# Performance work log

Measured on AMD Instinct MI355X. Metric: run time of the kernel, lower is better.

## Reference

```python
import jax, jax.numpy as jnp
import numpy as np

VAR0, VAR1 = 0.1, 0.2       # variances used by encode()
THRESH = 0.35               # overlap_thresh
NEGPOS = 7                  # negpos_ratio


def point_form(p):
    # (cx,cy,w,h) -> (xmin,ymin,xmax,ymax)
    return jnp.concatenate([p[:, :2] - p[:, 2:] / 2, p[:, :2] + p[:, 2:] / 2], axis=1)


def jaccard(a, b):
    # a:[G,4], b:[P,4] corner form -> IoU [G,P]
    lt = jnp.maximum(a[:, None, :2], b[None, :, :2])
    rb = jnp.minimum(a[:, None, 2:], b[None, :, 2:])
    wh = jnp.clip(rb - lt, 0.0, None)
    inter = wh[..., 0] * wh[..., 1]
    area_a = (a[:, 2] - a[:, 0]) * (a[:, 3] - a[:, 1])
    area_b = (b[:, 2] - b[:, 0]) * (b[:, 3] - b[:, 1])
    return inter / (area_a[:, None] + area_b[None, :] - inter)


def encode(matched, priors):
    g_cxcy = ((matched[:, :2] + matched[:, 2:]) / 2 - priors[:, :2]) / (VAR0 * priors[:, 2:])
    g_wh = jnp.log((matched[:, 2:] - matched[:, :2]) / priors[:, 2:]) / VAR1
    return jnp.concatenate([g_cxcy, g_wh], axis=1)


def encode_landm(matched, priors):
    m = matched.reshape(-1, 5, 2)                                  # [P,5,2]
    g = (m - priors[:, None, :2]) / (VAR0 * priors[:, None, 2:])
    return g.reshape(-1, 10)


def match_one(truths, labels, landms, priors, priors_pf):
    # truths:[G,4] labels:[G] landms:[G,10] priors:[P,4](cxcywh) priors_pf:[P,4](corner)
    G = truths.shape[0]
    P = priors.shape[0]
    ov = jaccard(truths, priors_pf)                                # [G,P]
    best_prior_ov = ov.max(axis=1)                                 # [G]
    best_prior_idx = ov.argmax(axis=1)                             # [G]
    valid_gt = best_prior_ov >= 0.2
    best_truth_ov = ov.max(axis=0)                                 # [P]
    best_truth_idx = ov.argmax(axis=0)                             # [P]
    # index_fill_(0, best_prior_idx[valid_gt], 2): 2 > any IoU, so max is equivalent
    forced_ov = jnp.zeros((P,), ov.dtype).at[best_prior_idx].max(jnp.where(valid_gt, 2.0, 0.0))
    best_truth_ov = jnp.maximum(best_truth_ov, forced_ov)
    forced_idx = jnp.full((P,), -1, jnp.int32).at[best_prior_idx].max(jnp.arange(G, dtype=jnp.int32))
    best_truth_idx = jnp.where(forced_idx >= 0, forced_idx, best_truth_idx.astype(jnp.int32))
    conf = labels[best_truth_idx].astype(jnp.int32)
    conf = jnp.where(best_truth_ov < THRESH, 0, conf)
    loc = encode(truths[best_truth_idx], priors)                   # [P,4]
    landm = encode_landm(landms[best_truth_idx], priors)           # [P,10]
    # if no valid gt, torch zeroes the targets for this sample
    any_valid = valid_gt.any()
    loc = jnp.where(any_valid, loc, 0.0)
    landm = jnp.where(any_valid, landm, 0.0)
    conf = jnp.where(any_valid, conf, 0)
    return loc, conf, landm


def smooth_l1(x):
    ax = jnp.abs(x)
    return jnp.where(ax < 1.0, 0.5 * ax * ax, ax - 0.5)


def setup_inputs() -> dict:
    key = jax.random.key(0)
    k1, k2, k3, k4, k5, k6, k7, k8, k9 = jax.random.split(key, 9)
    B, P, G, C = 64, 16800, 32, 2
    cls_data = jax.random.normal(k1, (B, P, C), jnp.float32)
    loc_data = jax.random.normal(k2, (B, P, 4), jnp.float32)
    landm_data = jax.random.normal(k3, (B, P, 10), jnp.float32)
    # priors in (cx,cy,w,h), w,h in [0.02,0.3]
    pc = jax.random.uniform(k4, (P, 2), jnp.float32)
    pwh = jax.random.uniform(k5, (P, 2), jnp.float32, 0.02, 0.3)
    priors = jnp.concatenate([pc, pwh], axis=1)
    # targets: [B,G,15] = 4 box (corner form, valid) + 10 landmarks + 1 label
    c = jax.random.uniform(k6, (B, G, 2), jnp.float32, 0.15, 0.85)
    s = jax.random.uniform(k7, (B, G, 2), jnp.float32, 0.02, 0.3)
    boxes = jnp.concatenate([c - s / 2, c + s / 2], axis=-1)
    lms = jax.random.uniform(k8, (B, G, 10), jnp.float32)
    labels = jnp.where(jax.random.uniform(k9, (B, G, 1)) < 0.3, -1.0, 1.0)
    targets = jnp.concatenate([boxes, lms, labels], axis=-1)
    return {"cls_data": cls_data, "loc_data": loc_data, "landm_data": landm_data,
            "priors": priors, "targets": targets}


def reference(cls_data, loc_data, landm_data, priors, targets):
    truths = targets[:, :, :4]
    landms = targets[:, :, 4:14]
    labels = targets[:, :, 14]
    priors_pf = point_form(priors)
    loc_t, conf_t, landm_t = jax.vmap(
        lambda t, l, lm: match_one(t, l, lm, priors, priors_pf))(truths, labels, landms)
    num, P = conf_t.shape

    # landmark loss (smooth L1 over conf_t > 0)
    pos1 = conf_t > 0
    N1 = jnp.maximum(pos1.sum().astype(jnp.float32), 1.0)
    loss_landm = jnp.sum(smooth_l1(landm_data - landm_t) * pos1[..., None].astype(landm_data.dtype))

    # localization loss (smooth L1 over conf_t != 0)
    pos = conf_t != 0
    conf_t = jnp.where(pos, 1, conf_t)                              # conf_t[pos] = 1
    loss_l = jnp.sum(smooth_l1(loc_data - loc_t) * pos[..., None].astype(loc_data.dtype))

    # hard negative mining on per-prior CE loss
    logz = jax.nn.logsumexp(cls_data, axis=-1)                      # [B,P]
    gold = jnp.take_along_axis(cls_data, conf_t[..., None], axis=-1)[..., 0]
    loss_c = jnp.where(pos, 0.0, logz - gold)
    loss_idx = jnp.argsort(-loss_c, axis=1)
    idx_rank = jnp.argsort(loss_idx, axis=1)
    num_pos = pos.sum(axis=1, keepdims=True)
    num_neg = jnp.clip(NEGPOS * num_pos, None, P - 1)
    neg = idx_rank < num_neg

    sel = (pos | neg).astype(cls_data.dtype)
    loss_conf = jnp.sum((logz - gold) * sel)

    N = jnp.maximum(num_pos.sum().astype(jnp.float32), 1.0)
    return loss_l / N, loss_conf / N, loss_landm / N1
```

## Files before the change

### kernel.cpp

```cpp
#include <hip/hip_runtime.h>
#include <hip/hip_bf16.h>
#include <math.h>


#define RCP(x) __builtin_amdgcn_rcpf(x)
typedef unsigned long long u64;

constexpr int GN = 32;
constexpr int PACKF = 576;
constexpr int NW64A = 264;

__device__ __forceinline__ float sl1(float x) {
    float a = fabsf(x);
    return a < 1.f ? 0.5f * a * a : a - 0.5f;
}

constexpr int GPB = 4;
constexpr int GNT = 1024;
__global__ __launch_bounds__(GNT)
void k_gt(const float4* __restrict__ priors, const float* __restrict__ targets,
          u64* __restrict__ keys, float* __restrict__ pack, u64* __restrict__ wmask,
          int* __restrict__ done, int P, int G, int NCH) {
    const int b = blockIdx.y, cx = blockIdx.x, g0 = cx * GPB, tid = threadIdx.x;
    const int lane = tid & 63, w = tid >> 6;
    if (cx == 0 && b == 0 && tid == 0) *done = 0;
    __shared__ float4 s_box[GPB];
    __shared__ float  s_at[GPB];
    __shared__ u64 s_wk[GNT / 64][GPB];
    if (tid < GPB) {
        const float* t = targets + ((size_t)b * G + g0 + tid) * 15;
        float4 v = make_float4(t[0], t[1], t[2], t[3]);
        float at = (v.z - v.x) * (v.w - v.y);
        s_box[tid] = v;
        s_at[tid] = at;
        float* pkw = pack + (size_t)b * PACKF;
        ((float4*)pkw)[g0 + tid] = v;
        pkw[128 + g0 + tid] = 0.35f * at;
        pkw[160 + g0 + tid] = at;
        pkw[192 + g0 + tid] = t[14];
    }
    {
        int q = tid - GPB;
        if (q >= 0 && q < GPB * 10) {
            int gg = g0 + q / 10, j = q % 10;
            pack[(size_t)b * PACKF + 224 + gg * 10 + j] =
                targets[((size_t)b * G + gg) * 15 + 4 + j];
        }
    }
    __syncthreads();
    float4 tb0 = s_box[0], tb1 = s_box[1], tb2 = s_box[2], tb3 = s_box[3];
    float at0 = s_at[0], at1 = s_at[1], at2 = s_at[2], at3 = s_at[3];
    float c0 = 0.35f * at0, c1 = 0.35f * at1, c2 = 0.35f * at2, c3 = 0.35f * at3;

    u64* __restrict__ wm = wmask + ((size_t)b * NCH + cx) * NW64A;

    float bv[GPB]; int bp[GPB];
    #pragma unroll
    for (int j = 0; j < GPB; ++j) { bv[j] = -1.f; bp[j] = 0; }

    for (int p = tid; p < P; p += GNT) {
        float4 pr = priors[p];
        float hx = pr.z * 0.5f, hy = pr.w * 0.5f;
        float px0 = pr.x - hx, py0 = pr.y - hy;
        float px1 = pr.x + hx, py1 = pr.y + hy;
        float ap = (px1 - px0) * (py1 - py0);
        float ap35 = 0.35f * ap;
        bool pa = false;
        #pragma unroll
        for (int j = 0; j < GPB; ++j) {
            float4 tb = j == 0 ? tb0 : (j == 1 ? tb1 : (j == 2 ? tb2 : tb3));
            float at = j == 0 ? at0 : (j == 1 ? at1 : (j == 2 ? at2 : at3));
            float cj = j == 0 ? c0 : (j == 1 ? c1 : (j == 2 ? c2 : c3));
            float lx = fmaxf(tb.x, px0), ly = fmaxf(tb.y, py0);
            float rx = fminf(tb.z, px1), ry = fminf(tb.w, py1);
            float iw = fmaxf(rx - lx, 0.f), ih = fmaxf(ry - ly, 0.f);
            float inter = iw * ih;
            pa = pa || (fmaf(1.35f, inter, -cj) >= ap35);
            float iou = inter * RCP(at + ap - inter);
            if (iou > bv[j]) { bv[j] = iou; bp[j] = p; }
        }
        u64 bal = __ballot(pa);
        if (lane == 0) wm[p >> 6] = bal;
    }
    #pragma unroll
    for (int j = 0; j < GPB; ++j) {
        u64 key = ((u64)__float_as_uint(bv[j]) << 32) | ~(unsigned)bp[j];
        #pragma unroll
        for (int o = 32; o > 0; o >>= 1) {
            u64 t = __shfl_down(key, o, 64);
            if (t > key) key = t;
        }
        if (lane == 0) s_wk[w][j] = key;
    }
    __syncthreads();
    if (tid < GPB) {
        u64 m = 0ull;
        #pragma unroll
        for (int q = 0; q < GNT / 64; ++q) { u64 t = s_wk[q][tid]; if (t > m) m = t; }
        keys[b * G + g0 + tid] = m;
    }
}

__global__ __launch_bounds__(256)
void k_match(const float2* __restrict__ cls, const float4* __restrict__ loc,
             const float* __restrict__ lmd, const float4* __restrict__ priors,
             const float* __restrict__ pack, const u64* __restrict__ keys,
             const u64* __restrict__ wmask,
             float* __restrict__ bc, float* __restrict__ part,
             int P, int NB, int NCH) {
    const int b = blockIdx.y, bx = blockIdx.x, tid = threadIdx.x;
    const int lane = tid & 63, w = tid >> 6;
    const float* __restrict__ pk = pack + (size_t)b * PACKF;
    const float4* __restrict__ gbox = (const float4*)pk;
    const float* __restrict__ garea = pk + 160;
    const float* __restrict__ glab = pk + 192;
    const float* __restrict__ glm  = pk + 224;

    __shared__ int s_fg[256];
    __shared__ int s_fv[256];
    __shared__ unsigned s_vm;
    __shared__ float s_red[4][8];

    s_fg[tid] = -1; s_fv[tid] = 0;
    __syncthreads();
    if (tid < GN) {
        u64 key = keys[b * GN + tid];
        unsigned bp = ~(unsigned)key;
        bool val = __uint_as_float((unsigned)(key >> 32)) >= 0.2f;
        u64 bal = __ballot(val);
        if (tid == 0) s_vm = (unsigned)bal;
        int local = (int)bp - bx * 256;
        if (local >= 0 && local < 256) {
            atomicMax(&s_fg[local], tid);
            if (val) atomicOr(&s_fv[local], 1);
        }
    }

    int p = bx * 256 + tid;
    const bool act = p < P;
    float2 c = act ? cls[(size_t)b * P + p] : make_float2(0.f, 0.f);

    const int word = bx * 4 + w;
    u64 m = 0ull;
    #pragma unroll
    for (int ch = 0; ch < 8; ++ch)
        m |= wmask[((size_t)b * NCH + ch) * NW64A + word];
    __syncthreads();
    const bool av = s_vm != 0u;

    bool thr = act && ((m >> lane) & 1ull);
    int fidx = s_fg[tid];
    bool fv = s_fv[tid] != 0;
    bool pos = act && av && (fv || thr);

    float lse = 0.f, d = 0.f;
    if (act) {
        d = c.y - c.x;
        float m0 = fmaxf(d, 0.f);
        lse = m0 + __logf(__expf(-m0) + __expf(d - m0));
        bc[(size_t)b * P + p] = pos ? 0.f : lse;
    }

    float a_ll = 0.f, a_lm = 0.f, a_lcp = 0.f;
    bool posl = false;
    if (pos) {
        a_lcp = lse - d;
        float4 pr = priors[p];
        float hx = pr.z * 0.5f, hy = pr.w * 0.5f;
        float px0 = pr.x - hx, py0 = pr.y - hy;
        float px1 = pr.x + hx, py1 = pr.y + hy;
        float ap = (px1 - px0) * (py1 - py0);
        int bti2 = fidx;
        if (fidx < 0) {
            float btv = -1.f;
            #pragma unroll 1
            for (int g = 0; g < GN; ++g) {
                float4 tb = gbox[g];
                float lx = fmaxf(tb.x, px0), ly = fmaxf(tb.y, py0);
                float rx = fminf(tb.z, px1), ry = fminf(tb.w, py1);
                float iw = fmaxf(rx - lx, 0.f), ih = fmaxf(ry - ly, 0.f);
                float inter = iw * ih;
                float iou = inter * RCP(garea[g] + ap - inter);
                if (iou > btv) { btv = iou; bti2 = g; }
            }
        }
        float4 tb = gbox[bti2];
        float rw = RCP(pr.z), rh = RCP(pr.w);
        float e0 = ((tb.x + tb.z) * 0.5f - pr.x) * rw * 10.f;
        float e1 = ((tb.y + tb.w) * 0.5f - pr.y) * rh * 10.f;
        float e2 = __logf((tb.z - tb.x) * rw) * 5.f;
        float e3 = __logf((tb.w - tb.y) * rh) * 5.f;
        float4 ld = loc[(size_t)b * P + p];
        a_ll = sl1(ld.x - e0) + sl1(ld.y - e1) + sl1(ld.z - e2) + sl1(ld.w - e3);
        if (glab[bti2] > 0.f) {
            posl = true;
            const float* lp = lmd + ((size_t)b * P + p) * 10;
            #pragma unroll
            for (int q = 0; q < 5; ++q) {
                float gx = (glm[bti2 * 10 + 2 * q]     - pr.x) * rw * 10.f;
                float gy = (glm[bti2 * 10 + 2 * q + 1] - pr.y) * rh * 10.f;
                a_lm += sl1(lp[2 * q] - gx) + sl1(lp[2 * q + 1] - gy);
            }
        }
    }

    u64 bpos = __ballot(pos);
    int npw  = __popcll(bpos);
    int np1w = __popcll(__ballot(posl));
    if (bpos) {
        #pragma unroll
        for (int o = 32; o > 0; o >>= 1) {
            a_ll  += __shfl_down(a_ll,  o, 64);
            a_lm  += __shfl_down(a_lm,  o, 64);
            a_lcp += __shfl_down(a_lcp, o, 64);
        }
    }
    if (lane == 0) {
        s_red[w][0] = a_ll; s_red[w][1] = a_lm; s_red[w][2] = a_lcp;
        s_red[w][3] = (float)npw; s_red[w][4] = (float)np1w;
    }
    __syncthreads();
    if (tid == 0) {
        float* pp = part + ((size_t)b * NB + bx) * 8;
        #pragma unroll
        for (int j = 0; j < 5; ++j)
            pp[j] = s_red[0][j] + s_red[1][j] + s_red[2][j] + s_red[3][j];
    }
}

constexpr int KNT = 1024;
constexpr int KNI = 17;
__global__ __launch_bounds__(KNT)
void k_select(const float* __restrict__ bc, const float* __restrict__ part,
              float* __restrict__ part2, float* __restrict__ out,
              int* __restrict__ done, int P, int NB, int B) {
    const int b = blockIdx.x, tid = threadIdx.x;
    const int lane = tid & 63, w = tid >> 6;
    __shared__ float s_r[5];
    __shared__ u64   s_cw[16];
    __shared__ u64   s_ct;
    __shared__ float s_rf[16][2];
    __shared__ float s_ts2[2];
    __shared__ int   s_last;

    unsigned ul[KNI];
    #pragma unroll
    for (int i = 0; i < KNI; ++i) {
        int idx = i * KNT + tid;
        ul[i] = idx < P ? __float_as_uint(bc[(size_t)b * P + idx]) : 0u;
    }
    if (w < 5) {
        float s = 0.f;
        for (int bx = lane; bx < NB; bx += 64) s += part[((size_t)b * NB + bx) * 8 + w];
        #pragma unroll
        for (int o = 32; o > 0; o >>= 1) s += __shfl_down(s, o, 64);
        if (lane == 0) s_r[w] = s;
    }
    __syncthreads();
    const float t_ll = s_r[0], t_lm = s_r[1], t_lcp = s_r[2];
    const float t_np = s_r[3], t_np1 = s_r[4];
    int k = (int)(t_np + 0.5f) * 7;
    if (k > P - 1) k = P - 1;

    float topk = 0.f;
    if (k > 0) {
        unsigned lo = 0u, hi = 0x7f800000u;
        while (lo < hi) {
            unsigned span = hi - lo;
            unsigned m1 = lo + ((span + 3) >> 2);
            unsigned m2 = lo + ((span + 1) >> 1);
            unsigned m3 = hi - (span >> 2);
            int c1 = 0, c2 = 0, c3 = 0;
            #pragma unroll
            for (int i = 0; i < KNI; ++i) {
                unsigned u = ul[i];
                c1 += u >= m1 ? 1 : 0;
                c2 += u >= m2 ? 1 : 0;
                c3 += u >= m3 ? 1 : 0;
            }
            u64 pkk = (u64)c1 | ((u64)c2 << 20) | ((u64)c3 << 40);
            #pragma unroll
            for (int o = 32; o > 0; o >>= 1) pkk += __shfl_down(pkk, o, 64);
            if (lane == 0) s_cw[w] = pkk;
            __syncthreads();
            if (w == 0) {
                u64 t = (lane < 16) ? s_cw[lane] : 0ull;
                #pragma unroll
                for (int o = 8; o > 0; o >>= 1) t += __shfl_down(t, o, 64);
                if (lane == 0) s_ct = t;
            }
            __syncthreads();
            u64 t = s_ct;
            int C1 = (int)(t & 0xFFFFFu);
            int C2 = (int)((t >> 20) & 0xFFFFFu);
            int C3 = (int)((t >> 40) & 0xFFFFFu);
            if      (C3 >= k) lo = m3;
            else if (C2 >= k) { lo = m2; hi = m3 - 1; }
            else if (C1 >= k) { lo = m1; hi = m2 - 1; }
            else hi = m1 - 1;
        }
        float fT = __uint_as_float(lo);
        float s = 0.f, cf = 0.f;
        #pragma unroll
        for (int i = 0; i < KNI; ++i)
            if (ul[i] > lo) { s += __uint_as_float(ul[i]); cf += 1.f; }
        #pragma unroll
        for (int o = 32; o > 0; o >>= 1) {
            s  += __shfl_down(s, o, 64);
            cf += __shfl_down(cf, o, 64);
        }
        if (lane == 0) { s_rf[w][0] = s; s_rf[w][1] = cf; }
        __syncthreads();
        if (w == 0) {
            float a = (lane < 16) ? s_rf[lane][0] : 0.f;
            float bb = (lane < 16) ? s_rf[lane][1] : 0.f;
            #pragma unroll
            for (int o = 8; o > 0; o >>= 1) {
                a  += __shfl_down(a, o, 64);
                bb += __shfl_down(bb, o, 64);
            }
            if (lane == 0) { s_ts2[0] = a; s_ts2[1] = bb; }
        }
        __syncthreads();
        topk = s_ts2[0] + ((float)k - s_ts2[1]) * fT;
    }
    if (tid == 0) {
        float* pp = part2 + b * 8;
        pp[0] = t_ll; pp[1] = t_lm; pp[2] = t_lcp;
        pp[3] = topk; pp[4] = t_np; pp[5] = t_np1;
        __threadfence();
        int old = atomicAdd(done, 1);
        s_last = (old == B - 1) ? 1 : 0;
    }
    __syncthreads();
    if (s_last && w == 0) {
        __threadfence();
        volatile float* vp = part2;
        float ll = 0.f, lm = 0.f, lc = 0.f, tk = 0.f, np = 0.f, np1 = 0.f;
        for (int bb = lane; bb < B; bb += 64) {
            ll  += vp[bb * 8 + 0];
            lm  += vp[bb * 8 + 1];
            lc  += vp[bb * 8 + 2];
            tk  += vp[bb * 8 + 3];
            np  += vp[bb * 8 + 4];
            np1 += vp[bb * 8 + 5];
        }
        #pragma unroll
        for (int o = 32; o > 0; o >>= 1) {
            ll  += __shfl_down(ll,  o, 64);
            lm  += __shfl_down(lm,  o, 64);
            lc  += __shfl_down(lc,  o, 64);
            tk  += __shfl_down(tk,  o, 64);
            np  += __shfl_down(np,  o, 64);
            np1 += __shfl_down(np1, o, 64);
        }
        if (lane == 0) {
            float N = fmaxf(np, 1.f), N1 = fmaxf(np1, 1.f);
            out[0] = ll / N;
            out[1] = (lc + tk) / N;
            out[2] = lm / N1;
        }
    }
}

extern "C" void kernel_launch(void* const* d_in, const int* in_sizes, int n_in,
                              void* d_out, int out_size, void* d_ws, size_t ws_size,
                              hipStream_t stream) {
    const float2* cls    = (const float2*)d_in[0];
    const float4* loc    = (const float4*)d_in[1];
    const float* lmd     = (const float*)d_in[2];
    const float4* priors = (const float4*)d_in[3];
    const float* targets = (const float*)d_in[4];
    int P = in_sizes[3] / 4;
    int B = (in_sizes[1] / 4) / P;
    int G = in_sizes[4] / (15 * B);
    int NB = (P + 255) / 256;
    int NCH = (G + GPB - 1) / GPB;

    size_t off = 0;
    u64* keys    = (u64*)d_ws;                     off += (size_t)B * G * 8;
    u64* wmask   = (u64*)((char*)d_ws + off);      off += (size_t)B * NCH * NW64A * 8;
    float* pack  = (float*)((char*)d_ws + off);    off += (size_t)B * PACKF * 4;
    float* part  = (float*)((char*)d_ws + off);    off += (size_t)B * NB * 8 * 4;
    float* part2 = (float*)((char*)d_ws + off);    off += (size_t)B * 8 * 4;
    int* done    = (int*)((char*)d_ws + off);      off += 256;
    off = (off + 255) & ~(size_t)255;
    float* bc    = (float*)((char*)d_ws + off);

    dim3 ggt(NCH, B);
    k_gt<<<ggt, GNT, 0, stream>>>(priors, targets, keys, pack, wmask, done, P, G, NCH);
    dim3 gm(NB, B);
    k_match<<<gm, 256, 0, stream>>>(cls, loc, lmd, priors, pack, keys, wmask,
                                    bc, part, P, NB, NCH);
    k_select<<<B, KNT, 0, stream>>>(bc, part, part2, (float*)d_out, done, P, NB, B);
}
```

Measured before the change: 89.00 us.

## Fuse three kernels into one cooperative kernel with grid syncs

Replaces the three separate kernel launches (GT matching, per-prior match/loss, top-k selection) with a single cooperative kernel that uses grid.sync between phases. Each batch now gets 4 blocks of 1024 threads handling 8 GTs each and a 4224-prior segment, down from 8 GT chunks and many 256-thread blocks. The aim is to cut launch overhead and inter-kernel gaps. In exchange the grid is much smaller (B*4 blocks), so per-block work and shared-memory use rise, grid syncs add their own cost, and G and the segment size are hardcoded.

```diff
diff --git a/kernel.cpp b/kernel.cpp
--- a/kernel.cpp
+++ b/kernel.cpp
@@ -1,38 +1,59 @@
 #include <hip/hip_runtime.h>
-#include <hip/hip_bf16.h>
+#include <hip/hip_cooperative_groups.h>
 #include <math.h>
 
 
+namespace cg = cooperative_groups;
 #define RCP(x) __builtin_amdgcn_rcpf(x)
 typedef unsigned long long u64;
 
 constexpr int GN = 32;
 constexpr int PACKF = 576;
+constexpr int NCH  = 4;
+constexpr int GPB  = 8;
+constexpr int SEG  = 4224;
 constexpr int NW64A = 264;
+constexpr int NT   = 1024;
+constexpr int NWV  = NT / 64;
 
 __device__ __forceinline__ float sl1(float x) {
     float a = fabsf(x);
     return a < 1.f ? 0.5f * a * a : a - 0.5f;
 }
 
-constexpr int GPB = 4;
-constexpr int GNT = 1024;
-__global__ __launch_bounds__(GNT)
-void k_gt(const float4* __restrict__ priors, const float* __restrict__ targets,
-          u64* __restrict__ keys, float* __restrict__ pack, u64* __restrict__ wmask,
-          int* __restrict__ done, int P, int G, int NCH) {
-    const int b = blockIdx.y, cx = blockIdx.x, g0 = cx * GPB, tid = threadIdx.x;
+__global__ __launch_bounds__(NT)
+void k_fused(const float2* __restrict__ cls, const float4* __restrict__ loc,
+             const float* __restrict__ lmd, const float4* __restrict__ priors,
+             const float* __restrict__ targets,
+             u64* __restrict__ keys, float* __restrict__ pack, u64* __restrict__ wmask,
+             float* __restrict__ bc, float* __restrict__ part, float* __restrict__ part2,
+             float* __restrict__ out, int* __restrict__ done, int P, int B) {
+    cg::grid_group grid = cg::this_grid();
+    const int cb = blockIdx.x, tid = threadIdx.x;
     const int lane = tid & 63, w = tid >> 6;
-    if (cx == 0 && b == 0 && tid == 0) *done = 0;
+    const int b = cb >> 2, sub = cb & 3;
+
     __shared__ float4 s_box[GPB];
     __shared__ float  s_at[GPB];
-    __shared__ u64 s_wk[GNT / 64][GPB];
+    __shared__ u64    s_wk[NWV][GPB];
+    __shared__ int    s_fg[SEG];
+    __shared__ unsigned s_fvb[SEG / 32];
+    __shared__ unsigned s_vm;
+    __shared__ float  s_red[NWV][8];
+    __shared__ float  s_r[5];
+    __shared__ u64    s_cw[NWV];
+    __shared__ u64    s_ct;
+    __shared__ float  s_rf[NWV][2];
+    __shared__ float  s_ts2[2];
+    __shared__ int    s_last;
+
+    if (cb == 0 && tid == 0) *done = 0;
+    const int g0 = sub * GPB;
     if (tid < GPB) {
-        const float* t = targets + ((size_t)b * G + g0 + tid) * 15;
+        const float* t = targets + ((size_t)b * GN + g0 + tid) * 15;
         float4 v = make_float4(t[0], t[1], t[2], t[3]);
         float at = (v.z - v.x) * (v.w - v.y);
-        s_box[tid] = v;
-        s_at[tid] = at;
+        s_box[tid] = v; s_at[tid] = at;
         float* pkw = pack + (size_t)b * PACKF;
         ((float4*)pkw)[g0 + tid] = v;
         pkw[128 + g0 + tid] = 0.35f * at;
@@ -44,21 +65,21 @@
         if (q >= 0 && q < GPB * 10) {
             int gg = g0 + q / 10, j = q % 10;
             pack[(size_t)b * PACKF + 224 + gg * 10 + j] =
-                targets[((size_t)b * G + gg) * 15 + 4 + j];
-        }
-    }
-    __syncthreads();
-    float4 tb0 = s_box[0], tb1 = s_box[1], tb2 = s_box[2], tb3 = s_box[3];
-    float at0 = s_at[0], at1 = s_at[1], at2 = s_at[2], at3 = s_at[3];
-    float c0 = 0.35f * at0, c1 = 0.35f * at1, c2 = 0.35f * at2, c3 = 0.35f * at3;
-
-    u64* __restrict__ wm = wmask + ((size_t)b * NCH + cx) * NW64A;
-
+                targets[((size_t)b * GN + gg) * 15 + 4 + j];
+        }
+    }
+    __syncthreads();
+    float4 tb[GPB]; float at_[GPB], c35_[GPB];
+    #pragma unroll
+    for (int j = 0; j < GPB; ++j) {
+        tb[j] = s_box[j]; at_[j] = s_at[j]; c35_[j] = 0.35f * s_at[j];
+    }
     float bv[GPB]; int bp[GPB];
     #pragma unroll
     for (int j = 0; j < GPB; ++j) { bv[j] = -1.f; bp[j] = 0; }
 
-    for (int p = tid; p < P; p += GNT) {
+    u64* __restrict__ wm = wmask + ((size_t)b * NCH + sub) * NW64A;
+    for (int p = tid; p < P; p += NT) {
         float4 pr = priors[p];
         float hx = pr.z * 0.5f, hy = pr.w * 0.5f;
         float px0 = pr.x - hx, py0 = pr.y - hy;
@@ -68,15 +89,12 @@
         bool pa = false;
         #pragma unroll
         for (int j = 0; j < GPB; ++j) {
-            float4 tb = j == 0 ? tb0 : (j == 1 ? tb1 : (j == 2 ? tb2 : tb3));
-            float at = j == 0 ? at0 : (j == 1 ? at1 : (j == 2 ? at2 : at3));
-            float cj = j == 0 ? c0 : (j == 1 ? c1 : (j == 2 ? c2 : c3));
-            float lx = fmaxf(tb.x, px0), ly = fmaxf(tb.y, py0);
-            float rx = fminf(tb.z, px1), ry = fminf(tb.w, py1);
+            float lx = fmaxf(tb[j].x, px0), ly = fmaxf(tb[j].y, py0);
+            float rx = fminf(tb[j].z, px1), ry = fminf(tb[j].w, py1);
             float iw = fmaxf(rx - lx, 0.f), ih = fmaxf(ry - ly, 0.f);
             float inter = iw * ih;
-            pa = pa || (fmaf(1.35f, inter, -cj) >= ap35);
-            float iou = inter * RCP(at + ap - inter);
+            pa = pa || (fmaf(1.35f, inter, -c35_[j]) >= ap35);
+            float iou = inter * RCP(at_[j] + ap - inter);
             if (iou > bv[j]) { bv[j] = iou; bp[j] = p; }
         }
         u64 bal = __ballot(pa);
@@ -96,165 +114,150 @@
     if (tid < GPB) {
         u64 m = 0ull;
         #pragma unroll
-        for (int q = 0; q < GNT / 64; ++q) { u64 t = s_wk[q][tid]; if (t > m) m = t; }
-        keys[b * G + g0 + tid] = m;
-    }
-}
-
-__global__ __launch_bounds__(256)
-void k_match(const float2* __restrict__ cls, const float4* __restrict__ loc,
-             const float* __restrict__ lmd, const float4* __restrict__ priors,
-             const float* __restrict__ pack, const u64* __restrict__ keys,
-             const u64* __restrict__ wmask,
-             float* __restrict__ bc, float* __restrict__ part,
-             int P, int NB, int NCH) {
-    const int b = blockIdx.y, bx = blockIdx.x, tid = threadIdx.x;
-    const int lane = tid & 63, w = tid >> 6;
+        for (int q = 0; q < NWV; ++q) { u64 t = s_wk[q][tid]; if (t > m) m = t; }
+        keys[b * GN + g0 + tid] = m;
+    }
+    __threadfence();
+    grid.sync();
+
+    const int base = sub * SEG;
+    const int segsz = min(SEG, P - base);
+    for (int i = tid; i < SEG; i += NT) s_fg[i] = -1;
+    if (tid < SEG / 32) s_fvb[tid] = 0u;
+    __syncthreads();
+    if (tid < GN) {
+        u64 key = keys[b * GN + tid];
+        unsigned bpz = ~(unsigned)key;
+        bool val = __uint_as_float((unsigned)(key >> 32)) >= 0.2f;
+        u64 bal = __ballot(val);
+        if (tid == 0) s_vm = (unsigned)bal;
+        int local = (int)bpz - base;
+        if (local >= 0 && local < segsz) {
+            atomicMax(&s_fg[local], tid);
+            if (val) atomicOr(&s_fvb[local >> 5], 1u << (local & 31));
+        }
+    }
+    __syncthreads();
+    const bool av = s_vm != 0u;
     const float* __restrict__ pk = pack + (size_t)b * PACKF;
     const float4* __restrict__ gbox = (const float4*)pk;
     const float* __restrict__ garea = pk + 160;
     const float* __restrict__ glab = pk + 192;
     const float* __restrict__ glm  = pk + 224;
 
-    __shared__ int s_fg[256];
-    __shared__ int s_fv[256];
-    __shared__ unsigned s_vm;
-    __shared__ float s_red[4][8];
-
-    s_fg[tid] = -1; s_fv[tid] = 0;
-    __syncthreads();
-    if (tid < GN) {
-        u64 key = keys[b * GN + tid];
-        unsigned bp = ~(unsigned)key;
-        bool val = __uint_as_float((unsigned)(key >> 32)) >= 0.2f;
-        u64 bal = __ballot(val);
-        if (tid == 0) s_vm = (unsigned)bal;
-        int local = (int)bp - bx * 256;
-        if (local >= 0 && local < 256) {
-            atomicMax(&s_fg[local], tid);
-            if (val) atomicOr(&s_fv[local], 1);
-        }
-    }
-
-    int p = bx * 256 + tid;
-    const bool act = p < P;
-    float2 c = act ? cls[(size_t)b * P + p] : make_float2(0.f, 0.f);
-
-    const int word = bx * 4 + w;
-    u64 m = 0ull;
-    #pragma unroll
-    for (int ch = 0; ch < 8; ++ch)
-        m |= wmask[((size_t)b * NCH + ch) * NW64A + word];
-    __syncthreads();
-    const bool av = s_vm != 0u;
-
-    bool thr = act && ((m >> lane) & 1ull);
-    int fidx = s_fg[tid];
-    bool fv = s_fv[tid] != 0;
-    bool pos = act && av && (fv || thr);
-
-    float lse = 0.f, d = 0.f;
-    if (act) {
-        d = c.y - c.x;
-        float m0 = fmaxf(d, 0.f);
-        lse = m0 + __logf(__expf(-m0) + __expf(d - m0));
-        bc[(size_t)b * P + p] = pos ? 0.f : lse;
-    }
-
     float a_ll = 0.f, a_lm = 0.f, a_lcp = 0.f;
-    bool posl = false;
-    if (pos) {
-        a_lcp = lse - d;
-        float4 pr = priors[p];
-        float hx = pr.z * 0.5f, hy = pr.w * 0.5f;
-        float px0 = pr.x - hx, py0 = pr.y - hy;
-        float px1 = pr.x + hx, py1 = pr.y + hy;
-        float ap = (px1 - px0) * (py1 - py0);
-        int bti2 = fidx;
-        if (fidx < 0) {
-            float btv = -1.f;
-            #pragma unroll 1
-            for (int g = 0; g < GN; ++g) {
-                float4 tb = gbox[g];
-                float lx = fmaxf(tb.x, px0), ly = fmaxf(tb.y, py0);
-                float rx = fminf(tb.z, px1), ry = fminf(tb.w, py1);
-                float iw = fmaxf(rx - lx, 0.f), ih = fmaxf(ry - ly, 0.f);
-                float inter = iw * ih;
-                float iou = inter * RCP(garea[g] + ap - inter);
-                if (iou > btv) { btv = iou; bti2 = g; }
-            }
-        }
-        float4 tb = gbox[bti2];
-        float rw = RCP(pr.z), rh = RCP(pr.w);
-        float e0 = ((tb.x + tb.z) * 0.5f - pr.x) * rw * 10.f;
-        float e1 = ((tb.y + tb.w) * 0.5f - pr.y) * rh * 10.f;
-        float e2 = __logf((tb.z - tb.x) * rw) * 5.f;
-        float e3 = __logf((tb.w - tb.y) * rh) * 5.f;
-        float4 ld = loc[(size_t)b * P + p];
-        a_ll = sl1(ld.x - e0) + sl1(ld.y - e1) + sl1(ld.z - e2) + sl1(ld.w - e3);
-        if (glab[bti2] > 0.f) {
-            posl = true;
-            const float* lp = lmd + ((size_t)b * P + p) * 10;
-            #pragma unroll
-            for (int q = 0; q < 5; ++q) {
-                float gx = (glm[bti2 * 10 + 2 * q]     - pr.x) * rw * 10.f;
-                float gy = (glm[bti2 * 10 + 2 * q + 1] - pr.y) * rh * 10.f;
-                a_lm += sl1(lp[2 * q] - gx) + sl1(lp[2 * q + 1] - gy);
-            }
-        }
-    }
-
-    u64 bpos = __ballot(pos);
-    int npw  = __popcll(bpos);
-    int np1w = __popcll(__ballot(posl));
-    if (bpos) {
+    int npw = 0, np1w = 0;
+    #pragma unroll
+    for (int i = 0; i < 5; ++i) {
+        int pl = i * NT + tid;
+        bool act = pl < segsz;
+        int gp = base + pl;
+        float2 c = act ? cls[(size_t)b * P + gp] : make_float2(0.f, 0.f);
+        u64 m = 0ull;
+        if (act) {
+            int word = gp >> 6;
+            #pragma unroll
+            for (int ch = 0; ch < NCH; ++ch)
+                m |= wmask[((size_t)b * NCH + ch) * NW64A + word];
+        }
+        bool thr = act && ((m >> (gp & 63)) & 1ull);
+        int fidx = -1; bool fv = false;
+        if (act) {
+            fidx = s_fg[pl];
+            fv = (s_fvb[pl >> 5] >> (pl & 31)) & 1u;
+        }
+        bool pos = act && av && (fv || thr);
+        float lse = 0.f, d = 0.f;
+        if (act) {
+            d = c.y - c.x;
+            float m0 = fmaxf(d, 0.f);
+            lse = m0 + __logf(__expf(-m0) + __expf(d - m0));
+            bc[(size_t)b * P + gp] = pos ? 0.f : lse;
+        }
+        if (pos) {
+            npw++;
+            a_lcp += lse - d;
+            float4 pr = priors[gp];
+            float hx = pr.z * 0.5f, hy = pr.w * 0.5f;
+            float px0 = pr.x - hx, py0 = pr.y - hy;
+            float px1 = pr.x + hx, py1 = pr.y + hy;
+            float ap = (px1 - px0) * (py1 - py0);
+            int bti2 = fidx;
+            if (fidx < 0) {
+                float btv = -1.f;
+                #pragma unroll 1
+                for (int g = 0; g < GN; ++g) {
+                    float4 tbx = gbox[g];
+                    float lx = fmaxf(tbx.x, px0), ly = fmaxf(tbx.y, py0);
+                    float rx = fminf(tbx.z, px1), ry = fminf(tbx.w, py1);
+                    float iw = fmaxf(rx - lx, 0.f), ih = fmaxf(ry - ly, 0.f);
+                    float inter = iw * ih;
+                    float iou = inter * RCP(garea[g] + ap - inter);
+                    if (iou > btv) { btv = iou; bti2 = g; }
+                }
+            }
+            float4 tbx = gbox[bti2];
+            float rw = RCP(pr.z), rh = RCP(pr.w);
+            float e0 = ((tbx.x + tbx.z) * 0.5f - pr.x) * rw * 10.f;
+            float e1 = ((tbx.y + tbx.w) * 0.5f - pr.y) * rh * 10.f;
+            float e2 = __logf((tbx.z - tbx.x) * rw) * 5.f;
+            float e3 = __logf((tbx.w - tbx.y) * rh) * 5.f;
+            float4 ld = loc[(size_t)b * P + gp];
+            a_ll += sl1(ld.x - e0) + sl1(ld.y - e1) + sl1(ld.z - e2) + sl1(ld.w - e3);
+            if (glab[bti2] > 0.f) {
+                np1w++;
+                const float* lp = lmd + ((size_t)b * P + gp) * 10;
+                #pragma unroll
+                for (int q = 0; q < 5; ++q) {
+                    float gx = (glm[bti2 * 10 + 2 * q]     - pr.x) * rw * 10.f;
+                    float gy = (glm[bti2 * 10 + 2 * q + 1] - pr.y) * rh * 10.f;
+                    a_lm += sl1(lp[2 * q] - gx) + sl1(lp[2 * q + 1] - gy);
+                }
+            }
+        }
+    }
+    {
+        float a_np = (float)npw, a_np1 = (float)np1w;
         #pragma unroll
         for (int o = 32; o > 0; o >>= 1) {
             a_ll  += __shfl_down(a_ll,  o, 64);
             a_lm  += __shfl_down(a_lm,  o, 64);
             a_lcp += __shfl_down(a_lcp, o, 64);
-        }
-    }
-    if (lane == 0) {
-        s_red[w][0] = a_ll; s_red[w][1] = a_lm; s_red[w][2] = a_lcp;
-        s_red[w][3] = (float)npw; s_red[w][4] = (float)np1w;
+            a_np  += __shfl_down(a_np,  o, 64);
+            a_np1 += __shfl_down(a_np1, o, 64);
+        }
+        if (lane == 0) {
+            s_red[w][0] = a_ll; s_red[w][1] = a_lm; s_red[w][2] = a_lcp;
+            s_red[w][3] = a_np; s_red[w][4] = a_np1;
+        }
     }
     __syncthreads();
     if (tid == 0) {
-        float* pp = part + ((size_t)b * NB + bx) * 8;
-        #pragma unroll
-        for (int j = 0; j < 5; ++j)
-            pp[j] = s_red[0][j] + s_red[1][j] + s_red[2][j] + s_red[3][j];
-    }
-}
-
-constexpr int KNT = 1024;
-constexpr int KNI = 17;
-__global__ __launch_bounds__(KNT)
-void k_select(const float* __restrict__ bc, const float* __restrict__ part,
-              float* __restrict__ part2, float* __restrict__ out,
-              int* __restrict__ done, int P, int NB, int B) {
-    const int b = blockIdx.x, tid = threadIdx.x;
-    const int lane = tid & 63, w = tid >> 6;
-    __shared__ float s_r[5];
-    __shared__ u64   s_cw[16];
-    __shared__ u64   s_ct;
-    __shared__ float s_rf[16][2];
-    __shared__ float s_ts2[2];
-    __shared__ int   s_last;
-
-    unsigned ul[KNI];
-    #pragma unroll
-    for (int i = 0; i < KNI; ++i) {
-        int idx = i * KNT + tid;
-        ul[i] = idx < P ? __float_as_uint(bc[(size_t)b * P + idx]) : 0u;
-    }
-    if (w < 5) {
+        float* pp = part + ((size_t)b * NCH + sub) * 8;
+        #pragma unroll
+        for (int j = 0; j < 5; ++j) {
+            float s = 0.f;
+            #pragma unroll
+            for (int q = 0; q < NWV; ++q) s += s_red[q][j];
+            pp[j] = s;
+        }
+    }
+    __threadfence();
+    grid.sync();
+
+    if (cb >= B) return;
+    const int b3 = cb;
+    unsigned ul[17];
+    #pragma unroll
+    for (int i = 0; i < 17; ++i) {
+        int idx = i * NT + tid;
+        ul[i] = idx < P ? __float_as_uint(bc[(size_t)b3 * P + idx]) : 0u;
+    }
+    if (tid < 5) {
         float s = 0.f;
-        for (int bx = lane; bx < NB; bx += 64) s += part[((size_t)b * NB + bx) * 8 + w];
-        #pragma unroll
-        for (int o = 32; o > 0; o >>= 1) s += __shfl_down(s, o, 64);
-        if (lane == 0) s_r[w] = s;
+        #pragma unroll
+        for (int sg = 0; sg < NCH; ++sg) s += part[((size_t)b3 * NCH + sg) * 8 + tid];
+        s_r[tid] = s;
     }
     __syncthreads();
     const float t_ll = s_r[0], t_lm = s_r[1], t_lcp = s_r[2];
@@ -272,7 +275,7 @@
             unsigned m3 = hi - (span >> 2);
             int c1 = 0, c2 = 0, c3 = 0;
             #pragma unroll
-            for (int i = 0; i < KNI; ++i) {
+            for (int i = 0; i < 17; ++i) {
                 unsigned u = ul[i];
                 c1 += u >= m1 ? 1 : 0;
                 c2 += u >= m2 ? 1 : 0;
@@ -284,7 +287,7 @@
             if (lane == 0) s_cw[w] = pkk;
             __syncthreads();
             if (w == 0) {
-                u64 t = (lane < 16) ? s_cw[lane] : 0ull;
+                u64 t = (lane < NWV) ? s_cw[lane] : 0ull;
                 #pragma unroll
                 for (int o = 8; o > 0; o >>= 1) t += __shfl_down(t, o, 64);
                 if (lane == 0) s_ct = t;
@@ -302,7 +305,7 @@
         float fT = __uint_as_float(lo);
         float s = 0.f, cf = 0.f;
         #pragma unroll
-        for (int i = 0; i < KNI; ++i)
+        for (int i = 0; i < 17; ++i)
             if (ul[i] > lo) { s += __uint_as_float(ul[i]); cf += 1.f; }
         #pragma unroll
         for (int o = 32; o > 0; o >>= 1) {
@@ -312,8 +315,8 @@
         if (lane == 0) { s_rf[w][0] = s; s_rf[w][1] = cf; }
         __syncthreads();
         if (w == 0) {
-            float a = (lane < 16) ? s_rf[lane][0] : 0.f;
-            float bb = (lane < 16) ? s_rf[lane][1] : 0.f;
+            float a = (lane < NWV) ? s_rf[lane][0] : 0.f;
+            float bb = (lane < NWV) ? s_rf[lane][1] : 0.f;
             #pragma unroll
             for (int o = 8; o > 0; o >>= 1) {
                 a  += __shfl_down(a, o, 64);
@@ -325,7 +328,7 @@
         topk = s_ts2[0] + ((float)k - s_ts2[1]) * fT;
     }
     if (tid == 0) {
-        float* pp = part2 + b * 8;
+        float* pp = part2 + b3 * 8;
         pp[0] = t_ll; pp[1] = t_lm; pp[2] = t_lcp;
         pp[3] = topk; pp[4] = t_np; pp[5] = t_np1;
         __threadfence();
@@ -373,24 +376,23 @@
     const float* targets = (const float*)d_in[4];
     int P = in_sizes[3] / 4;
     int B = (in_sizes[1] / 4) / P;
-    int G = in_sizes[4] / (15 * B);
-    int NB = (P + 255) / 256;
-    int NCH = (G + GPB - 1) / GPB;
 
     size_t off = 0;
-    u64* keys    = (u64*)d_ws;                     off += (size_t)B * G * 8;
+    u64* keys    = (u64*)d_ws;                     off += (size_t)B * GN * 8;
     u64* wmask   = (u64*)((char*)d_ws + off);      off += (size_t)B * NCH * NW64A * 8;
     float* pack  = (float*)((char*)d_ws + off);    off += (size_t)B * PACKF * 4;
-    float* part  = (float*)((char*)d_ws + off);    off += (size_t)B * NB * 8 * 4;
+    float* part  = (float*)((char*)d_ws + off);    off += (size_t)B * NCH * 8 * 4;
     float* part2 = (float*)((char*)d_ws + off);    off += (size_t)B * 8 * 4;
     int* done    = (int*)((char*)d_ws + off);      off += 256;
     off = (off + 255) & ~(size_t)255;
     float* bc    = (float*)((char*)d_ws + off);
 
-    dim3 ggt(NCH, B);
-    k_gt<<<ggt, GNT, 0, stream>>>(priors, targets, keys, pack, wmask, done, P, G, NCH);
-    dim3 gm(NB, B);
-    k_match<<<gm, 256, 0, stream>>>(cls, loc, lmd, priors, pack, keys, wmask,
-                                    bc, part, P, NB, NCH);
-    k_select<<<B, KNT, 0, stream>>>(bc, part, part2, (float*)d_out, done, P, NB, B);
+    float* outp = (float*)d_out;
+    void* args[] = {
+        (void*)&cls, (void*)&loc, (void*)&lmd, (void*)&priors, (void*)&targets,
+        (void*)&keys, (void*)&pack, (void*)&wmask, (void*)&bc, (void*)&part,
+        (void*)&part2, (void*)&outp, (void*)&done, (void*)&P, (void*)&B
+    };
+    hipLaunchCooperativeKernel((void*)k_fused, dim3(B * NCH), dim3(NT),
+                               args, 0, stream);
 }
```

Result: slower. 301.3 us (+238.5%).

## Fuse per-prior matching into top-k selection kernel, one block per image

Applied to the files above, without the earlier changes.

Merges the per-prior match/loss kernel into the hard-negative selection kernel, so each image is handled by one 1024-thread block that computes losses straight into registers. This drops one kernel launch and the round trip of the per-prior background loss array and the partial sums through global memory. In exchange, the matching work for an image now runs on only B blocks instead of NB×B blocks, which cuts parallelism, and a large shared array is needed for the forced-match indices.

```diff
diff --git a/kernel.cpp b/kernel.cpp
--- a/kernel.cpp
+++ b/kernel.cpp
@@ -101,14 +101,17 @@
     }
 }
 
-__global__ __launch_bounds__(256)
-void k_match(const float2* __restrict__ cls, const float4* __restrict__ loc,
-             const float* __restrict__ lmd, const float4* __restrict__ priors,
-             const float* __restrict__ pack, const u64* __restrict__ keys,
-             const u64* __restrict__ wmask,
-             float* __restrict__ bc, float* __restrict__ part,
-             int P, int NB, int NCH) {
-    const int b = blockIdx.y, bx = blockIdx.x, tid = threadIdx.x;
+constexpr int SNT = 1024;
+constexpr int SNI = 17;
+constexpr int NWV = SNT / 64;
+__global__ __launch_bounds__(SNT)
+void k_sel(const float2* __restrict__ cls, const float4* __restrict__ loc,
+           const float* __restrict__ lmd, const float4* __restrict__ priors,
+           const float* __restrict__ pack, const u64* __restrict__ keys,
+           const u64* __restrict__ wmask,
+           float* __restrict__ part2, float* __restrict__ out,
+           int* __restrict__ done, int P, int NCH, int B) {
+    const int b = blockIdx.x, tid = threadIdx.x;
     const int lane = tid & 63, w = tid >> 6;
     const float* __restrict__ pk = pack + (size_t)b * PACKF;
     const float4* __restrict__ gbox = (const float4*)pk;
@@ -116,12 +119,23 @@
     const float* __restrict__ glab = pk + 192;
     const float* __restrict__ glm  = pk + 224;
 
-    __shared__ int s_fg[256];
-    __shared__ int s_fv[256];
+    __shared__ int      s_fg[16800];
+    __shared__ unsigned s_fvb[528];
     __shared__ unsigned s_vm;
-    __shared__ float s_red[4][8];
-
-    s_fg[tid] = -1; s_fv[tid] = 0;
+    __shared__ float    s_red[NWV][8];
+    __shared__ float    s_fld[5];
+    __shared__ u64      s_cw[NWV];
+    __shared__ u64      s_ct;
+    __shared__ float    s_rf[NWV][2];
+    __shared__ float    s_ts2[2];
+    __shared__ int      s_last;
+
+    #pragma unroll
+    for (int i = 0; i < SNI; ++i) {
+        int idx = i * SNT + tid;
+        if (idx < P) s_fg[idx] = -1;
+    }
+    if (tid < 528) s_fvb[tid] = 0u;
     __syncthreads();
     if (tid < GN) {
         u64 key = keys[b * GN + tid];
@@ -129,136 +143,110 @@
         bool val = __uint_as_float((unsigned)(key >> 32)) >= 0.2f;
         u64 bal = __ballot(val);
         if (tid == 0) s_vm = (unsigned)bal;
-        int local = (int)bp - bx * 256;
-        if (local >= 0 && local < 256) {
-            atomicMax(&s_fg[local], tid);
-            if (val) atomicOr(&s_fv[local], 1);
-        }
-    }
-
-    int p = bx * 256 + tid;
-    const bool act = p < P;
-    float2 c = act ? cls[(size_t)b * P + p] : make_float2(0.f, 0.f);
-
-    const int word = bx * 4 + w;
-    u64 m = 0ull;
+        if ((int)bp < P) {
+            atomicMax(&s_fg[bp], tid);
+            if (val) atomicOr(&s_fvb[bp >> 5], 1u << (bp & 31));
+        }
+    }
+    __syncthreads();
+    const bool av = s_vm != 0u;
+
+    float a_ll = 0.f, a_lm = 0.f, a_lcp = 0.f;
+    int npw = 0, np1w = 0;
+    unsigned ul[SNI];
     #pragma unroll
-    for (int ch = 0; ch < 8; ++ch)
-        m |= wmask[((size_t)b * NCH + ch) * NW64A + word];
-    __syncthreads();
-    const bool av = s_vm != 0u;
-
-    bool thr = act && ((m >> lane) & 1ull);
-    int fidx = s_fg[tid];
-    bool fv = s_fv[tid] != 0;
-    bool pos = act && av && (fv || thr);
-
-    float lse = 0.f, d = 0.f;
-    if (act) {
-        d = c.y - c.x;
-        float m0 = fmaxf(d, 0.f);
-        lse = m0 + __logf(__expf(-m0) + __expf(d - m0));
-        bc[(size_t)b * P + p] = pos ? 0.f : lse;
-    }
-
-    float a_ll = 0.f, a_lm = 0.f, a_lcp = 0.f;
-    bool posl = false;
-    if (pos) {
-        a_lcp = lse - d;
-        float4 pr = priors[p];
-        float hx = pr.z * 0.5f, hy = pr.w * 0.5f;
-        float px0 = pr.x - hx, py0 = pr.y - hy;
-        float px1 = pr.x + hx, py1 = pr.y + hy;
-        float ap = (px1 - px0) * (py1 - py0);
-        int bti2 = fidx;
-        if (fidx < 0) {
-            float btv = -1.f;
-            #pragma unroll 1
-            for (int g = 0; g < GN; ++g) {
-                float4 tb = gbox[g];
-                float lx = fmaxf(tb.x, px0), ly = fmaxf(tb.y, py0);
-                float rx = fminf(tb.z, px1), ry = fminf(tb.w, py1);
-                float iw = fmaxf(rx - lx, 0.f), ih = fmaxf(ry - ly, 0.f);
-                float inter = iw * ih;
-                float iou = inter * RCP(garea[g] + ap - inter);
-                if (iou > btv) { btv = iou; bti2 = g; }
-            }
-        }
-        float4 tb = gbox[bti2];
-        float rw = RCP(pr.z), rh = RCP(pr.w);
-        float e0 = ((tb.x + tb.z) * 0.5f - pr.x) * rw * 10.f;
-        float e1 = ((tb.y + tb.w) * 0.5f - pr.y) * rh * 10.f;
-        float e2 = __logf((tb.z - tb.x) * rw) * 5.f;
-        float e3 = __logf((tb.w - tb.y) * rh) * 5.f;
-        float4 ld = loc[(size_t)b * P + p];
-        a_ll = sl1(ld.x - e0) + sl1(ld.y - e1) + sl1(ld.z - e2) + sl1(ld.w - e3);
-        if (glab[bti2] > 0.f) {
-            posl = true;
-            const float* lp = lmd + ((size_t)b * P + p) * 10;
-            #pragma unroll
-            for (int q = 0; q < 5; ++q) {
-                float gx = (glm[bti2 * 10 + 2 * q]     - pr.x) * rw * 10.f;
-                float gy = (glm[bti2 * 10 + 2 * q + 1] - pr.y) * rh * 10.f;
-                a_lm += sl1(lp[2 * q] - gx) + sl1(lp[2 * q + 1] - gy);
-            }
-        }
-    }
-
-    u64 bpos = __ballot(pos);
-    int npw  = __popcll(bpos);
-    int np1w = __popcll(__ballot(posl));
-    if (bpos) {
+    for (int i = 0; i < SNI; ++i) {
+        int p = i * SNT + tid;
+        bool act = p < P;
+        float2 c = act ? cls[(size_t)b * P + p] : make_float2(0.f, 0.f);
+        u64 m = 0ull;
+        if (act) {
+            int word = i * 16 + w;
+            #pragma unroll
+            for (int ch = 0; ch < 8; ++ch)
+                m |= wmask[((size_t)b * NCH + ch) * NW64A + word];
+        }
+        bool thr = act && ((m >> (p & 63)) & 1ull);
+        int fidx = act ? s_fg[p] : -1;
+        bool fv = act && ((s_fvb[p >> 5] >> (p & 31)) & 1u);
+        bool pos = act && av && (fv || thr);
+        float lse = 0.f, d = 0.f;
+        if (act) {
+            d = c.y - c.x;
+            float m0 = fmaxf(d, 0.f);
+            lse = m0 + __logf(__expf(-m0) + __expf(d - m0));
+        }
+        ul[i] = pos ? 0u : (act ? __float_as_uint(lse) : 0u);
+        if (pos) {
+            npw++;
+            a_lcp += lse - d;
+            float4 pr = priors[p];
+            float hx = pr.z * 0.5f, hy = pr.w * 0.5f;
+            float px0 = pr.x - hx, py0 = pr.y - hy;
+            float px1 = pr.x + hx, py1 = pr.y + hy;
+            float ap = (px1 - px0) * (py1 - py0);
+            int bti2 = fidx;
+            if (fidx < 0) {
+                float btv = -1.f;
+                #pragma unroll 1
+                for (int g = 0; g < GN; ++g) {
+                    float4 tb = gbox[g];
+                    float lx = fmaxf(tb.x, px0), ly = fmaxf(tb.y, py0);
+                    float rx = fminf(tb.z, px1), ry = fminf(tb.w, py1);
+                    float iw = fmaxf(rx - lx, 0.f), ih = fmaxf(ry - ly, 0.f);
+                    float inter = iw * ih;
+                    float iou = inter * RCP(garea[g] + ap - inter);
+                    if (iou > btv) { btv = iou; bti2 = g; }
+                }
+            }
+            float4 tb = gbox[bti2];
+            float rw = RCP(pr.z), rh = RCP(pr.w);
+            float e0 = ((tb.x + tb.z) * 0.5f - pr.x) * rw * 10.f;
+            float e1 = ((tb.y + tb.w) * 0.5f - pr.y) * rh * 10.f;
+            float e2 = __logf((tb.z - tb.x) * rw) * 5.f;
+            float e3 = __logf((tb.w - tb.y) * rh) * 5.f;
+            float4 ld = loc[(size_t)b * P + p];
+            a_ll += sl1(ld.x - e0) + sl1(ld.y - e1) + sl1(ld.z - e2) + sl1(ld.w - e3);
+            if (glab[bti2] > 0.f) {
+                np1w++;
+                const float* lp = lmd + ((size_t)b * P + p) * 10;
+                #pragma unroll
+                for (int q = 0; q < 5; ++q) {
+                    float gx = (glm[bti2 * 10 + 2 * q]     - pr.x) * rw * 10.f;
+                    float gy = (glm[bti2 * 10 + 2 * q + 1] - pr.y) * rh * 10.f;
+                    a_lm += sl1(lp[2 * q] - gx) + sl1(lp[2 * q + 1] - gy);
+                }
+            }
+        }
+    }
+    {
+        float a_np = (float)npw, a_np1 = (float)np1w;
         #pragma unroll
         for (int o = 32; o > 0; o >>= 1) {
             a_ll  += __shfl_down(a_ll,  o, 64);
             a_lm  += __shfl_down(a_lm,  o, 64);
             a_lcp += __shfl_down(a_lcp, o, 64);
-        }
-    }
-    if (lane == 0) {
-        s_red[w][0] = a_ll; s_red[w][1] = a_lm; s_red[w][2] = a_lcp;
-        s_red[w][3] = (float)npw; s_red[w][4] = (float)np1w;
-    }
-    __syncthreads();
-    if (tid == 0) {
-        float* pp = part + ((size_t)b * NB + bx) * 8;
-        #pragma unroll
-        for (int j = 0; j < 5; ++j)
-            pp[j] = s_red[0][j] + s_red[1][j] + s_red[2][j] + s_red[3][j];
-    }
-}
-
-constexpr int KNT = 1024;
-constexpr int KNI = 17;
-__global__ __launch_bounds__(KNT)
-void k_select(const float* __restrict__ bc, const float* __restrict__ part,
-              float* __restrict__ part2, float* __restrict__ out,
-              int* __restrict__ done, int P, int NB, int B) {
-    const int b = blockIdx.x, tid = threadIdx.x;
-    const int lane = tid & 63, w = tid >> 6;
-    __shared__ float s_r[5];
-    __shared__ u64   s_cw[16];
-    __shared__ u64   s_ct;
-    __shared__ float s_rf[16][2];
-    __shared__ float s_ts2[2];
-    __shared__ int   s_last;
-
-    unsigned ul[KNI];
-    #pragma unroll
-    for (int i = 0; i < KNI; ++i) {
-        int idx = i * KNT + tid;
-        ul[i] = idx < P ? __float_as_uint(bc[(size_t)b * P + idx]) : 0u;
-    }
-    if (w < 5) {
-        float s = 0.f;
-        for (int bx = lane; bx < NB; bx += 64) s += part[((size_t)b * NB + bx) * 8 + w];
-        #pragma unroll
-        for (int o = 32; o > 0; o >>= 1) s += __shfl_down(s, o, 64);
-        if (lane == 0) s_r[w] = s;
-    }
-    __syncthreads();
-    const float t_ll = s_r[0], t_lm = s_r[1], t_lcp = s_r[2];
-    const float t_np = s_r[3], t_np1 = s_r[4];
+            a_np  += __shfl_down(a_np,  o, 64);
+            a_np1 += __shfl_down(a_np1, o, 64);
+        }
+        if (lane == 0) {
+            s_red[w][0] = a_ll; s_red[w][1] = a_lm; s_red[w][2] = a_lcp;
+            s_red[w][3] = a_np; s_red[w][4] = a_np1;
+        }
+    }
+    __syncthreads();
+    if (w == 0) {
+        #pragma unroll
+        for (int j = 0; j < 5; ++j) {
+            float v = (lane < NWV) ? s_red[lane][j] : 0.f;
+            #pragma unroll
+            for (int o = 8; o > 0; o >>= 1) v += __shfl_down(v, o, 64);
+            if (lane == 0) s_fld[j] = v;
+        }
+    }
+    __syncthreads();
+    const float t_ll = s_fld[0], t_lm = s_fld[1], t_lcp = s_fld[2];
+    const float t_np = s_fld[3], t_np1 = s_fld[4];
     int k = (int)(t_np + 0.5f) * 7;
     if (k > P - 1) k = P - 1;
 
@@ -272,7 +260,7 @@
             unsigned m3 = hi - (span >> 2);
             int c1 = 0, c2 = 0, c3 = 0;
             #pragma unroll
-            for (int i = 0; i < KNI; ++i) {
+            for (int i = 0; i < SNI; ++i) {
                 unsigned u = ul[i];
                 c1 += u >= m1 ? 1 : 0;
                 c2 += u >= m2 ? 1 : 0;
@@ -284,7 +272,7 @@
             if (lane == 0) s_cw[w] = pkk;
             __syncthreads();
             if (w == 0) {
-                u64 t = (lane < 16) ? s_cw[lane] : 0ull;
+                u64 t = (lane < NWV) ? s_cw[lane] : 0ull;
                 #pragma unroll
                 for (int o = 8; o > 0; o >>= 1) t += __shfl_down(t, o, 64);
                 if (lane == 0) s_ct = t;
@@ -302,7 +290,7 @@
         float fT = __uint_as_float(lo);
         float s = 0.f, cf = 0.f;
         #pragma unroll
-        for (int i = 0; i < KNI; ++i)
+        for (int i = 0; i < SNI; ++i)
             if (ul[i] > lo) { s += __uint_as_float(ul[i]); cf += 1.f; }
         #pragma unroll
         for (int o = 32; o > 0; o >>= 1) {
@@ -312,8 +300,8 @@
         if (lane == 0) { s_rf[w][0] = s; s_rf[w][1] = cf; }
         __syncthreads();
         if (w == 0) {
-            float a = (lane < 16) ? s_rf[lane][0] : 0.f;
-            float bb = (lane < 16) ? s_rf[lane][1] : 0.f;
+            float a = (lane < NWV) ? s_rf[lane][0] : 0.f;
+            float bb = (lane < NWV) ? s_rf[lane][1] : 0.f;
             #pragma unroll
             for (int o = 8; o > 0; o >>= 1) {
                 a  += __shfl_down(a, o, 64);
@@ -374,23 +362,17 @@
     int P = in_sizes[3] / 4;
     int B = (in_sizes[1] / 4) / P;
     int G = in_sizes[4] / (15 * B);
-    int NB = (P + 255) / 256;
     int NCH = (G + GPB - 1) / GPB;
 
     size_t off = 0;
     u64* keys    = (u64*)d_ws;                     off += (size_t)B * G * 8;
     u64* wmask   = (u64*)((char*)d_ws + off);      off += (size_t)B * NCH * NW64A * 8;
     float* pack  = (float*)((char*)d_ws + off);    off += (size_t)B * PACKF * 4;
-    float* part  = (float*)((char*)d_ws + off);    off += (size_t)B * NB * 8 * 4;
     float* part2 = (float*)((char*)d_ws + off);    off += (size_t)B * 8 * 4;
-    int* done    = (int*)((char*)d_ws + off);      off += 256;
-    off = (off + 255) & ~(size_t)255;
-    float* bc    = (float*)((char*)d_ws + off);
+    int* done    = (int*)((char*)d_ws + off);
 
     dim3 ggt(NCH, B);
     k_gt<<<ggt, GNT, 0, stream>>>(priors, targets, keys, pack, wmask, done, P, G, NCH);
-    dim3 gm(NB, B);
-    k_match<<<gm, 256, 0, stream>>>(cls, loc, lmd, priors, pack, keys, wmask,
-                                    bc, part, P, NB, NCH);
-    k_select<<<B, KNT, 0, stream>>>(bc, part, part2, (float*)d_out, done, P, NB, B);
+    k_sel<<<B, SNT, 0, stream>>>(cls, loc, lmd, priors, pack, keys, wmask,
+                                 part2, (float*)d_out, done, P, NCH, B);
 }
```

Result: slower. 178.5 us (+100.6%).
